# Kernel tuning notes

Hardware: AMD Instinct MI355X
Metric: run time of the kernel (lower is better)

Reference implementation:

```python
import jax, jax.numpy as jnp
import numpy as np

D_MODEL = 1024
N_HEADS = 16
D_HEAD = D_MODEL // N_HEADS
D_FF = 4096
B, L = 4, 2048


def setup_inputs() -> dict:
    key = jax.random.key(0)
    ks = jax.random.split(key, 12)
    s = 0.02
    return {
        "x": jax.random.normal(ks[0], (B, L, D_MODEL), dtype=jnp.float32),
        "ln1_g": jnp.ones((D_MODEL,), jnp.float32),
        "ln1_b": jnp.zeros((D_MODEL,), jnp.float32),
        "w_qkv": jax.random.normal(ks[1], (D_MODEL, 3 * D_MODEL), jnp.float32) * s,
        "b_qkv": jnp.zeros((3 * D_MODEL,), jnp.float32),
        "w_out": jax.random.normal(ks[2], (D_MODEL, D_MODEL), jnp.float32) * s,
        "b_out": jnp.zeros((D_MODEL,), jnp.float32),
        "ln2_g": jnp.ones((D_MODEL,), jnp.float32),
        "ln2_b": jnp.zeros((D_MODEL,), jnp.float32),
        "w1": jax.random.normal(ks[3], (D_MODEL, D_FF), jnp.float32) * s,
        "b1": jnp.zeros((D_FF,), jnp.float32),
        "w2": jax.random.normal(ks[4], (D_FF, D_MODEL), jnp.float32) * s,
        "b2": jnp.zeros((D_MODEL,), jnp.float32),
    }


def _layernorm(x, g, b, eps=1e-5):
    mu = jnp.mean(x, axis=-1, keepdims=True)
    var = jnp.var(x, axis=-1, keepdims=True)
    return (x - mu) * jax.lax.rsqrt(var + eps) * g + b


def _attention(h, w_qkv, b_qkv, w_out, b_out):
    Bx, Lx, D = h.shape
    qkv = h @ w_qkv + b_qkv  # [B,L,3D]
    qkv = qkv.reshape(Bx, Lx, 3, N_HEADS, D_HEAD)
    q, k, v = qkv[:, :, 0], qkv[:, :, 1], qkv[:, :, 2]  # [B,L,H,Dh]
    att = jnp.einsum("bqhd,bkhd->bhqk", q, k) * (D_HEAD ** -0.5)
    causal = jnp.tril(jnp.ones((Lx, Lx), bool))
    att = jnp.where(causal, att, -jnp.inf)
    att = jax.nn.softmax(att, axis=-1)
    out = jnp.einsum("bhqk,bkhd->bqhd", att, v).reshape(Bx, Lx, D)
    return out @ w_out + b_out


def reference(x, ln1_g, ln1_b, w_qkv, b_qkv, w_out, b_out,
              ln2_g, ln2_b, w1, b1, w2, b2):
    h = x + _attention(_layernorm(x, ln1_g, ln1_b), w_qkv, b_qkv, w_out, b_out)
    ff = jax.nn.gelu(_layernorm(h, ln2_g, ln2_b) @ w1 + b1, approximate=False) @ w2 + b2
    return h + ff
```

## Files before the change

### kernel.cpp

```cpp
#include <hip/hip_runtime.h>
#include <hip/hip_bf16.h>


typedef float f32x4 __attribute__((ext_vector_type(4)));
typedef __bf16 bf16x8 __attribute__((ext_vector_type(8)));
typedef unsigned short u16;

#define MFMA16(a, b, c) __builtin_amdgcn_mfma_f32_16x16x32_bf16((a), (b), (c), 0, 0, 0)

#define GLL16(g, l)                                                            \
  __builtin_amdgcn_global_load_lds(                                            \
      (__attribute__((address_space(1))) void*)(g),                            \
      (__attribute__((address_space(3))) void*)(l), 16, 0, 0)

__device__ __forceinline__ u16 f2bf(float f) {
  union { float f; unsigned int u; } x; x.f = f;
  unsigned int r = x.u + 0x7fffu + ((x.u >> 16) & 1u);
  return (u16)(r >> 16);
}

__global__ __launch_bounds__(256) void ln_kernel(
    const float* __restrict__ x, const float* __restrict__ g,
    const float* __restrict__ b, u16* __restrict__ y)
{
  int row = blockIdx.x;
  int t = threadIdx.x;
  const float4* xr = (const float4*)(x + (size_t)row * 1024);
  float4 v = xr[t];
  float s  = v.x + v.y + v.z + v.w;
  float ss = v.x*v.x + v.y*v.y + v.z*v.z + v.w*v.w;
#pragma unroll
  for (int off = 1; off < 64; off <<= 1) {
    s  += __shfl_xor(s, off);
    ss += __shfl_xor(ss, off);
  }
  __shared__ float red[8];
  int w = t >> 6;
  if ((t & 63) == 0) { red[w*2] = s; red[w*2+1] = ss; }
  __syncthreads();
  s  = red[0] + red[2] + red[4] + red[6];
  ss = red[1] + red[3] + red[5] + red[7];
  float mu  = s * (1.0f / 1024.0f);
  float var = ss * (1.0f / 1024.0f) - mu * mu;
  float rs  = rsqrtf(var + 1e-5f);
  float4 gg = ((const float4*)g)[t];
  float4 bb = ((const float4*)b)[t];
  ushort4 o;
  o.x = f2bf((v.x - mu) * rs * gg.x + bb.x);
  o.y = f2bf((v.y - mu) * rs * gg.y + bb.y);
  o.z = f2bf((v.z - mu) * rs * gg.z + bb.z);
  o.w = f2bf((v.w - mu) * rs * gg.w + bb.w);
  ((ushort4*)y)[(size_t)row * 256 + t] = o;
}

__global__ __launch_bounds__(256) void wt_kernel(
    const float* __restrict__ W, u16* __restrict__ Wt, int K, int N)
{
  __shared__ u16 tile[32][33];
  int n0 = blockIdx.x * 32, k0 = blockIdx.y * 32;
  int t = threadIdx.x, tr = t >> 5, tc = t & 31;
#pragma unroll
  for (int i = 0; i < 4; ++i) {
    int k = k0 + tr + i * 8;
    tile[tc][tr + i * 8] = f2bf(W[(size_t)k * N + n0 + tc]);
  }
  __syncthreads();
#pragma unroll
  for (int i = 0; i < 4; ++i) {
    int n = n0 + tr + i * 8;
    Wt[(size_t)n * K + k0 + tc] = tile[tr + i * 8][tc];
  }
}

__global__ __launch_bounds__(256) void vt_kernel(
    const u16* __restrict__ qkv, u16* __restrict__ vt)
{
  __shared__ u16 tile[64][65];
  int bid = blockIdx.x;
  int lt = bid & 31, h = (bid >> 5) & 15, b = bid >> 9;
  int t = threadIdx.x;
  int tr = t >> 4, tc4 = (t & 15) * 4;
  const u16* src = qkv + ((size_t)(b * 2048 + lt * 64)) * 3072 + 2048 + h * 64;
#pragma unroll
  for (int i = 0; i < 4; ++i) {
    int ll = tr + i * 16;
    ushort4 v = *(const ushort4*)(src + (size_t)ll * 3072 + tc4);
    tile[ll][tc4] = v.x; tile[ll][tc4+1] = v.y; tile[ll][tc4+2] = v.z; tile[ll][tc4+3] = v.w;
  }
  __syncthreads();
  u16* dst = vt + ((size_t)(b * 16 + h) * 64) * 2048 + lt * 64;
#pragma unroll
  for (int i = 0; i < 4; ++i) {
    int d = tr + i * 16;
    ushort4 o;
    o.x = tile[tc4][d]; o.y = tile[tc4+1][d]; o.z = tile[tc4+2][d]; o.w = tile[tc4+3][d];
    *(ushort4*)(dst + (size_t)d * 2048 + tc4) = o;
  }
}

template<int GELU, int HAS_RES, int OUT_BF16>
__global__ __launch_bounds__(256, 2) void gemm_kernel(
    const u16* __restrict__ A, const u16* __restrict__ Bt,
    const float* __restrict__ bias, const float* __restrict__ res,
    void* __restrict__ Cout, int M, int N, int K)
{
  __shared__ u16 lA[3][128 * 32];
  __shared__ u16 lB[3][128 * 32];
  const int nbn = N >> 7;
  int nwg = gridDim.x;
  int wg = blockIdx.x;
  if ((nwg & 7) == 0) wg = (wg & 7) * (nwg >> 3) + (wg >> 3);
  int bm = wg / nbn, bn = wg % nbn;
  int tid = threadIdx.x;
  int w = tid >> 6, l = tid & 63;
  int lh = l & 15, lg = l >> 4;
  int wr = w >> 1, wc = w & 1;
  const size_t Kb = (size_t)K * 2;
  const char* Ab = (const char*)A + (size_t)(bm * 128) * Kb;
  const char* Bb = (const char*)Bt + (size_t)(bn * 128) * Kb;

  int c0 = w * 64 + l;
  int r0 = c0 >> 2, sw0 = ((c0 ^ (c0 >> 3)) & 3) << 4;
  int c1 = (4 + w) * 64 + l;
  int r1 = c1 >> 2, sw1 = ((c1 ^ (c1 >> 3)) & 3) << 4;

#define GSTAGE(sel, kt)                                                        \
  do {                                                                         \
    GLL16(Ab + (size_t)r0 * Kb + (size_t)(kt) * 64 + sw0,                      \
          (char*)lA[sel] + w * 1024);                                          \
    GLL16(Bb + (size_t)r0 * Kb + (size_t)(kt) * 64 + sw0,                      \
          (char*)lB[sel] + w * 1024);                                          \
    GLL16(Ab + (size_t)r1 * Kb + (size_t)(kt) * 64 + sw1,                      \
          (char*)lA[sel] + (4 + w) * 1024);                                    \
    GLL16(Bb + (size_t)r1 * Kb + (size_t)(kt) * 64 + sw1,                      \
          (char*)lB[sel] + (4 + w) * 1024);                                    \
  } while (0)

  const int swo = ((lg ^ (lh >> 1)) & 3) << 4;
  const int offA = (wr * 64 + lh) * 64 + swo;
  const int offB = (wc * 64 + lh) * 64 + swo;

  f32x4 acc[4][4] = {};
  const int nkt = K >> 5;
  GSTAGE(0, 0);
  GSTAGE(1, 1);
  asm volatile("s_waitcnt vmcnt(4)" ::: "memory");
  __builtin_amdgcn_s_barrier();
  __builtin_amdgcn_sched_barrier(0);

  int cur = 0, s2 = 2;
#pragma unroll 1
  for (int t = 0; t < nkt; ++t) {
    const char* bufA = (const char*)lA[cur];
    const char* bufB = (const char*)lB[cur];
    bf16x8 af[4], bfr[4];
#pragma unroll
    for (int m = 0; m < 4; ++m)
      af[m] = *(const bf16x8*)(bufA + offA + m * 1024);
#pragma unroll
    for (int n = 0; n < 4; ++n)
      bfr[n] = *(const bf16x8*)(bufB + offB + n * 1024);
    if (t + 2 < nkt) GSTAGE(s2, t + 2);
    __builtin_amdgcn_s_setprio(1);
#pragma unroll
    for (int m = 0; m < 4; ++m)
#pragma unroll
      for (int n = 0; n < 4; ++n)
        acc[m][n] = MFMA16(af[m], bfr[n], acc[m][n]);
    __builtin_amdgcn_s_setprio(0);
    if (t < nkt - 1) {
      __builtin_amdgcn_sched_barrier(0);
      if (t < nkt - 2) asm volatile("s_waitcnt vmcnt(4)" ::: "memory");
      else             asm volatile("s_waitcnt vmcnt(0)" ::: "memory");
      __builtin_amdgcn_s_barrier();
      __builtin_amdgcn_sched_barrier(0);
    }
    cur = (cur == 2) ? 0 : cur + 1;
    s2  = (s2 == 2) ? 0 : s2 + 1;
  }
#undef GSTAGE

#pragma unroll
  for (int m = 0; m < 4; ++m) {
    int row0 = bm * 128 + wr * 64 + m * 16 + lg * 4;
#pragma unroll
    for (int n = 0; n < 4; ++n) {
      int col = bn * 128 + wc * 64 + n * 16 + lh;
      float bv = bias[col];
#pragma unroll
      for (int r = 0; r < 4; ++r) {
        int row = row0 + r;
        float v = acc[m][n][r] + bv;
        if (GELU) v = 0.5f * v * (1.0f + erff(v * 0.70710678118f));
        if (HAS_RES) v += res[(size_t)row * N + col];
        if (OUT_BF16) ((u16*)Cout)[(size_t)row * N + col] = f2bf(v);
        else ((float*)Cout)[(size_t)row * N + col] = v;
      }
    }
  }
  (void)M;
}

__global__ __launch_bounds__(256, 4) void attn_kernel(
    const u16* __restrict__ qkv, const u16* __restrict__ vt,
    u16* __restrict__ out)
{
  __shared__ u16 Ks[2][4096];
  __shared__ u16 Vs[2][4096];
  __shared__ u16 Ps[4][1024];

  const float C = 0.18033688011f;

  int bid = blockIdx.x;
  int pi = bid >> 6, bh = bid & 63;
  int b = bh >> 4, h = bh & 15;
  int tid = threadIdx.x;
  int w = tid >> 6, l = tid & 63;
  int lh = l & 15, lg = l >> 4;
  int lh7 = lh & 7;

  const char* kg = (const char*)qkv + (size_t)(b * 2048) * 6144 + 2048 + h * 128;
  const char* vg = (const char*)vt + (size_t)((b * 16 + h) * 64) * 4096;
  char* pbw = (char*)Ps[w] + lh * 128;

#pragma unroll 1
  for (int half = 0; half < 2; ++half) {
    int qb = half ? (31 - pi) : pi;
    int q0 = qb * 64 + w * 16;
    const u16* qbase = qkv + ((size_t)(b * 2048) + q0) * 3072 + h * 64;
    bf16x8 aq0 = *(const bf16x8*)(qbase + (size_t)lh * 3072 + lg * 8);
    bf16x8 aq1 = *(const bf16x8*)(qbase + (size_t)lh * 3072 + 32 + lg * 8);

    f32x4 o[4] = {};
    float m = -1e30f;
    float lsum = 0.f;
    int nt = qb + 1;

    __syncthreads();
#pragma unroll
    for (int i = 0; i < 2; ++i) {
      int u = tid + i * 256;
      int row = u >> 3, uc = u & 7, sw = uc ^ (row & 7);
      GLL16(kg + (size_t)row * 6144 + sw * 16,
            (char*)Ks[0] + (size_t)(i * 256 + w * 64) * 16);
      GLL16(vg + (size_t)row * 4096 + sw * 16,
            (char*)Vs[0] + (size_t)(i * 256 + w * 64) * 16);
    }

#pragma unroll 1
    for (int kt = 0; kt < nt; ++kt) {
      int cur = kt & 1;
      __syncthreads();
      if (kt + 1 < nt) {
        int nxt = cur ^ 1;
        size_t kofs = (size_t)(kt + 1) * 64;
#pragma unroll
        for (int i = 0; i < 2; ++i) {
          int u = tid + i * 256;
          int row = u >> 3, uc = u & 7, sw = uc ^ (row & 7);
          GLL16(kg + (kofs + row) * 6144 + sw * 16,
                (char*)Ks[nxt] + (size_t)(i * 256 + w * 64) * 16);
          GLL16(vg + (size_t)row * 4096 + kofs * 2 + sw * 16,
                (char*)Vs[nxt] + (size_t)(i * 256 + w * 64) * 16);
        }
      }
      const char* kbuf = (const char*)Ks[cur];
      f32x4 s[4];
#pragma unroll
      for (int kb = 0; kb < 4; ++kb) {
        int row = kb * 16 + lh;
        const char* rp = kbuf + row * 128;
        bf16x8 a0 = *(const bf16x8*)(rp + ((lg ^ lh7) << 4));
        bf16x8 a1 = *(const bf16x8*)(rp + (((4 + lg) ^ lh7) << 4));
        f32x4 z = {0.f, 0.f, 0.f, 0.f};
        z = MFMA16(a0, aq0, z);
        z = MFMA16(a1, aq1, z);
        s[kb] = z;
      }
      if (kt == qb) {
        int qin = w * 16 + lh;
#pragma unroll
        for (int kb = 0; kb < 4; ++kb)
#pragma unroll
          for (int r = 0; r < 4; ++r)
            if (kb * 16 + lg * 4 + r > qin) s[kb][r] = -1e30f;
      }
      float tm = fmaxf(fmaxf(s[0][0], s[0][1]), fmaxf(s[0][2], s[0][3]));
#pragma unroll
      for (int kb = 1; kb < 4; ++kb)
        tm = fmaxf(tm, fmaxf(fmaxf(s[kb][0], s[kb][1]), fmaxf(s[kb][2], s[kb][3])));
      tm = fmaxf(tm, __shfl_xor(tm, 16));
      tm = fmaxf(tm, __shfl_xor(tm, 32));
      if (__any(tm > m + 64.0f)) {
        float nm = fmaxf(m, tm);
        float f = __builtin_amdgcn_exp2f((m - nm) * C);
        m = nm; lsum *= f;
#pragma unroll
        for (int db = 0; db < 4; ++db)
#pragma unroll
          for (int r = 0; r < 4; ++r) o[db][r] *= f;
      }
      float mc = m * C;
      float ps = 0.f;
#pragma unroll
      for (int kb = 0; kb < 4; ++kb)
#pragma unroll
        for (int r = 0; r < 4; ++r) {
          float p = __builtin_amdgcn_exp2f(fmaf(s[kb][r], C, -mc));
          s[kb][r] = p;
          ps += p;
        }
      ps += __shfl_xor(ps, 16);
      ps += __shfl_xor(ps, 32);
      lsum += ps;
#pragma unroll
      for (int kb = 0; kb < 4; ++kb) {
        unsigned lo, hi;
        asm("v_cvt_pk_bf16_f32 %0, %1, %2" : "=v"(lo) : "v"(s[kb][0]), "v"(s[kb][1]));
        asm("v_cvt_pk_bf16_f32 %0, %1, %2" : "=v"(hi) : "v"(s[kb][2]), "v"(s[kb][3]));
        int unit = kb * 2 + (lg >> 1);
        uint2 val; val.x = lo; val.y = hi;
        *(uint2*)(pbw + ((unit ^ lh7) << 4) + ((lg & 1) << 3)) = val;
      }
      bf16x8 pa0 = *(const bf16x8*)(pbw + ((lg ^ lh7) << 4));
      bf16x8 pa1 = *(const bf16x8*)(pbw + (((4 + lg) ^ lh7) << 4));
      const char* vbuf = (const char*)Vs[cur];
#pragma unroll
      for (int db = 0; db < 4; ++db) {
        int row = db * 16 + lh;
        const char* rp = vbuf + row * 128;
        bf16x8 v0 = *(const bf16x8*)(rp + ((lg ^ lh7) << 4));
        bf16x8 v1 = *(const bf16x8*)(rp + (((4 + lg) ^ lh7) << 4));
        o[db] = MFMA16(v0, pa0, o[db]);
        o[db] = MFMA16(v1, pa1, o[db]);
      }
    }
    float rinv = 1.0f / lsum;
    u16* ob = out + ((size_t)(b * 2048) + q0 + lh) * 1024 + h * 64;
#pragma unroll
    for (int db = 0; db < 4; ++db) {
      ushort4 pk;
      pk.x = f2bf(o[db][0] * rinv);
      pk.y = f2bf(o[db][1] * rinv);
      pk.z = f2bf(o[db][2] * rinv);
      pk.w = f2bf(o[db][3] * rinv);
      *(ushort4*)(ob + db * 16 + lg * 4) = pk;
    }
  }
}

extern "C" void kernel_launch(void* const* d_in, const int* in_sizes, int n_in,
                              void* d_out, int out_size, void* d_ws, size_t ws_size,
                              hipStream_t stream) {
  const float* x     = (const float*)d_in[0];
  const float* ln1_g = (const float*)d_in[1];
  const float* ln1_b = (const float*)d_in[2];
  const float* w_qkv = (const float*)d_in[3];
  const float* b_qkv = (const float*)d_in[4];
  const float* w_out = (const float*)d_in[5];
  const float* b_out = (const float*)d_in[6];
  const float* ln2_g = (const float*)d_in[7];
  const float* ln2_b = (const float*)d_in[8];
  const float* w1    = (const float*)d_in[9];
  const float* b1    = (const float*)d_in[10];
  const float* w2    = (const float*)d_in[11];
  const float* b2    = (const float*)d_in[12];

  char* ws = (char*)d_ws;
  u16* wqkvT = (u16*)(ws + 0);
  u16* woutT = (u16*)(ws + 6291456);
  u16* w1T   = (u16*)(ws + 8388608);
  u16* w2T   = (u16*)(ws + 16777216);
  u16* qkv   = (u16*)(ws + 25165824);
  u16* ffn1  = (u16*)(ws + 25165824);
  u16* vtb   = (u16*)(ws + 75497472);
  u16* lnb   = (u16*)(ws + 92274688);
  u16* attn  = lnb;
  float* h   = (float*)(ws + 125829120);

  wt_kernel<<<dim3(96, 32), 256, 0, stream>>>(w_qkv, wqkvT, 1024, 3072);
  wt_kernel<<<dim3(32, 32), 256, 0, stream>>>(w_out, woutT, 1024, 1024);
  wt_kernel<<<dim3(128, 32), 256, 0, stream>>>(w1, w1T, 1024, 4096);
  wt_kernel<<<dim3(32, 128), 256, 0, stream>>>(w2, w2T, 4096, 1024);

  ln_kernel<<<8192, 256, 0, stream>>>(x, ln1_g, ln1_b, lnb);
  gemm_kernel<0, 0, 1><<<1536, 256, 0, stream>>>(lnb, wqkvT, b_qkv, nullptr, qkv, 8192, 3072, 1024);
  vt_kernel<<<2048, 256, 0, stream>>>(qkv, vtb);
  attn_kernel<<<1024, 256, 0, stream>>>(qkv, vtb, attn);
  gemm_kernel<0, 1, 0><<<512, 256, 0, stream>>>(attn, woutT, b_out, x, h, 8192, 1024, 1024);
  ln_kernel<<<8192, 256, 0, stream>>>(h, ln2_g, ln2_b, lnb);
  gemm_kernel<1, 0, 1><<<2048, 256, 0, stream>>>(lnb, w1T, b1, nullptr, ffn1, 8192, 4096, 1024);
  gemm_kernel<0, 1, 0><<<512, 256, 0, stream>>>(ffn1, w2T, b2, h, (float*)d_out, 8192, 1024, 4096);
}
```

Baseline: 390.8 us.

## Enlarge GEMM tiles to 256-row blocks with 512 threads and 4-stage pipeline

The GEMM kernel moves from 128x128 tiles with 256 threads to 256xBN tiles (BN of 256 or 128) with 8 waves of 512 threads. It also deepens the LDS ring buffer from 3 to 4 stages with prefetch distance 3, adjusting the vmcnt waits to match. Larger tiles raise arithmetic intensity per global and LDS load and halve the grid sizes. The cost is more LDS per block (up to 128KB at BN=256), more accumulator registers, and possibly lower occupancy or fewer blocks than CUs for the N=1024 GEMMs.

After: 398.6 us. +2.0%, slower.

```diff
diff --git a/kernel.cpp b/kernel.cpp
--- a/kernel.cpp
+++ b/kernel.cpp
@@ -98,15 +98,19 @@
   }
 }
 
-template<int GELU, int HAS_RES, int OUT_BF16>
-__global__ __launch_bounds__(256, 2) void gemm_kernel(
+template<int BN, int GELU, int HAS_RES, int OUT_BF16>
+__global__ __launch_bounds__(512, 2) void gemm_kernel(
     const u16* __restrict__ A, const u16* __restrict__ Bt,
     const float* __restrict__ bias, const float* __restrict__ res,
     void* __restrict__ Cout, int M, int N, int K)
 {
-  __shared__ u16 lA[3][128 * 32];
-  __shared__ u16 lB[3][128 * 32];
-  const int nbn = N >> 7;
+  constexpr int WGN = BN / 64;
+  constexpr int MW  = (WGN == 4) ? 8 : 4;
+  constexpr int LPT = (BN == 256) ? 4 : 3;
+  __shared__ u16 lA[4][256 * 32];
+  __shared__ u16 lB[4][BN * 32];
+
+  const int nbn = N / BN;
   int nwg = gridDim.x;
   int wg = blockIdx.x;
   if ((nwg & 7) == 0) wg = (wg & 7) * (nwg >> 3) + (wg >> 3);
@@ -114,78 +118,80 @@
   int tid = threadIdx.x;
   int w = tid >> 6, l = tid & 63;
   int lh = l & 15, lg = l >> 4;
-  int wr = w >> 1, wc = w & 1;
+  int wr = w / WGN, wc = w % WGN;
   const size_t Kb = (size_t)K * 2;
-  const char* Ab = (const char*)A + (size_t)(bm * 128) * Kb;
-  const char* Bb = (const char*)Bt + (size_t)(bn * 128) * Kb;
-
-  int c0 = w * 64 + l;
-  int r0 = c0 >> 2, sw0 = ((c0 ^ (c0 >> 3)) & 3) << 4;
-  int c1 = (4 + w) * 64 + l;
-  int r1 = c1 >> 2, sw1 = ((c1 ^ (c1 >> 3)) & 3) << 4;
+  const char* Ab = (const char*)A + (size_t)(bm * 256) * Kb;
+  const char* Bb = (const char*)Bt + (size_t)(bn * BN) * Kb;
+
+  const int swst = ((tid ^ (tid >> 3)) & 3) << 4;
+  const size_t stR0 = (size_t)(tid >> 2) * Kb + swst;
+  const size_t stR1 = stR0 + 128 * Kb;
 
 #define GSTAGE(sel, kt)                                                        \
   do {                                                                         \
-    GLL16(Ab + (size_t)r0 * Kb + (size_t)(kt) * 64 + sw0,                      \
-          (char*)lA[sel] + w * 1024);                                          \
-    GLL16(Bb + (size_t)r0 * Kb + (size_t)(kt) * 64 + sw0,                      \
-          (char*)lB[sel] + w * 1024);                                          \
-    GLL16(Ab + (size_t)r1 * Kb + (size_t)(kt) * 64 + sw1,                      \
-          (char*)lA[sel] + (4 + w) * 1024);                                    \
-    GLL16(Bb + (size_t)r1 * Kb + (size_t)(kt) * 64 + sw1,                      \
-          (char*)lB[sel] + (4 + w) * 1024);                                    \
+    GLL16(Ab + stR0 + (size_t)(kt) * 64, (char*)lA[sel] + tid * 16);           \
+    GLL16(Ab + stR1 + (size_t)(kt) * 64, (char*)lA[sel] + tid * 16 + 8192);    \
+    GLL16(Bb + stR0 + (size_t)(kt) * 64, (char*)lB[sel] + tid * 16);           \
+    if (BN == 256)                                                             \
+      GLL16(Bb + stR1 + (size_t)(kt) * 64, (char*)lB[sel] + tid * 16 + 8192);  \
   } while (0)
 
   const int swo = ((lg ^ (lh >> 1)) & 3) << 4;
-  const int offA = (wr * 64 + lh) * 64 + swo;
+  const int offA = (wr * (MW * 16) + lh) * 64 + swo;
   const int offB = (wc * 64 + lh) * 64 + swo;
 
-  f32x4 acc[4][4] = {};
+  f32x4 acc[MW][4] = {};
   const int nkt = K >> 5;
   GSTAGE(0, 0);
   GSTAGE(1, 1);
-  asm volatile("s_waitcnt vmcnt(4)" ::: "memory");
+  GSTAGE(2, 2);
+  if (BN == 256) asm volatile("s_waitcnt vmcnt(8)" ::: "memory");
+  else           asm volatile("s_waitcnt vmcnt(6)" ::: "memory");
   __builtin_amdgcn_s_barrier();
   __builtin_amdgcn_sched_barrier(0);
 
-  int cur = 0, s2 = 2;
 #pragma unroll 1
   for (int t = 0; t < nkt; ++t) {
-    const char* bufA = (const char*)lA[cur];
-    const char* bufB = (const char*)lB[cur];
-    bf16x8 af[4], bfr[4];
-#pragma unroll
-    for (int m = 0; m < 4; ++m)
+    const char* bufA = (const char*)lA[t & 3];
+    const char* bufB = (const char*)lB[t & 3];
+    bf16x8 af[MW], bfr[4];
+#pragma unroll
+    for (int m = 0; m < MW; ++m)
       af[m] = *(const bf16x8*)(bufA + offA + m * 1024);
 #pragma unroll
     for (int n = 0; n < 4; ++n)
       bfr[n] = *(const bf16x8*)(bufB + offB + n * 1024);
-    if (t + 2 < nkt) GSTAGE(s2, t + 2);
+    if (t + 3 < nkt) GSTAGE((t + 3) & 3, t + 3);
     __builtin_amdgcn_s_setprio(1);
 #pragma unroll
-    for (int m = 0; m < 4; ++m)
+    for (int m = 0; m < MW; ++m)
 #pragma unroll
       for (int n = 0; n < 4; ++n)
         acc[m][n] = MFMA16(af[m], bfr[n], acc[m][n]);
     __builtin_amdgcn_s_setprio(0);
     if (t < nkt - 1) {
       __builtin_amdgcn_sched_barrier(0);
-      if (t < nkt - 2) asm volatile("s_waitcnt vmcnt(4)" ::: "memory");
-      else             asm volatile("s_waitcnt vmcnt(0)" ::: "memory");
+      if (t < nkt - 3) {
+        if (BN == 256) asm volatile("s_waitcnt vmcnt(8)" ::: "memory");
+        else           asm volatile("s_waitcnt vmcnt(6)" ::: "memory");
+      } else if (t == nkt - 3) {
+        if (BN == 256) asm volatile("s_waitcnt vmcnt(4)" ::: "memory");
+        else           asm volatile("s_waitcnt vmcnt(3)" ::: "memory");
+      } else {
+        asm volatile("s_waitcnt vmcnt(0)" ::: "memory");
+      }
       __builtin_amdgcn_s_barrier();
       __builtin_amdgcn_sched_barrier(0);
     }
-    cur = (cur == 2) ? 0 : cur + 1;
-    s2  = (s2 == 2) ? 0 : s2 + 1;
   }
 #undef GSTAGE
 
 #pragma unroll
-  for (int m = 0; m < 4; ++m) {
-    int row0 = bm * 128 + wr * 64 + m * 16 + lg * 4;
+  for (int m = 0; m < MW; ++m) {
+    int row0 = bm * 256 + wr * (MW * 16) + m * 16 + lg * 4;
 #pragma unroll
     for (int n = 0; n < 4; ++n) {
-      int col = bn * 128 + wc * 64 + n * 16 + lh;
+      int col = bn * BN + wc * 64 + n * 16 + lh;
       float bv = bias[col];
 #pragma unroll
       for (int r = 0; r < 4; ++r) {
@@ -384,11 +390,11 @@
   wt_kernel<<<dim3(32, 128), 256, 0, stream>>>(w2, w2T, 4096, 1024);
 
   ln_kernel<<<8192, 256, 0, stream>>>(x, ln1_g, ln1_b, lnb);
-  gemm_kernel<0, 0, 1><<<1536, 256, 0, stream>>>(lnb, wqkvT, b_qkv, nullptr, qkv, 8192, 3072, 1024);
+  gemm_kernel<256, 0, 0, 1><<<384, 512, 0, stream>>>(lnb, wqkvT, b_qkv, nullptr, qkv, 8192, 3072, 1024);
   vt_kernel<<<2048, 256, 0, stream>>>(qkv, vtb);
   attn_kernel<<<1024, 256, 0, stream>>>(qkv, vtb, attn);
-  gemm_kernel<0, 1, 0><<<512, 256, 0, stream>>>(attn, woutT, b_out, x, h, 8192, 1024, 1024);
+  gemm_kernel<128, 0, 1, 0><<<256, 512, 0, stream>>>(attn, woutT, b_out, x, h, 8192, 1024, 1024);
   ln_kernel<<<8192, 256, 0, stream>>>(h, ln2_g, ln2_b, lnb);
-  gemm_kernel<1, 0, 1><<<2048, 256, 0, stream>>>(lnb, w1T, b1, nullptr, ffn1, 8192, 4096, 1024);
-  gemm_kernel<0, 1, 0><<<512, 256, 0, stream>>>(ffn1, w2T, b2, h, (float*)d_out, 8192, 1024, 4096);
-}
+  gemm_kernel<256, 1, 0, 1><<<512, 512, 0, stream>>>(lnb, w1T, b1, nullptr, ffn1, 8192, 4096, 1024);
+  gemm_kernel<128, 0, 1, 0><<<256, 512, 0, stream>>>(ffn1, w2T, b2, h, (float*)d_out, 8192, 1024, 4096);
+}
```
